# Performance work log

Measured on AMD Instinct MI355X. Metric: run time of the kernel, lower is better.

Reference implementation:

```python
import jax, jax.numpy as jnp
import numpy as np

B, IN, OUT, K = 2048, 1024, 1024, 20


def setup_inputs() -> dict:
    key = jax.random.key(0)
    k1, k2 = jax.random.split(key)
    x = jax.random.normal(k1, (B, IN), dtype=jnp.float32)
    # per-output, per-input spline coefficients: (out_features, in_features, num_knots)
    W = jax.random.normal(k2, (OUT, IN, K), dtype=jnp.float32) * 0.1
    # evenly spaced knot grid on [-2, 2] (linspace)
    knots = jnp.linspace(-2.0, 2.0, K, dtype=jnp.float32)
    return {"x": x, "W": W, "knots": knots}


def reference(x, W, knots):
    # RBF spline basis shared across all output features (this is the fusion
    # the original per-output Python loop misses):
    # basis[b, i, k] = exp(-0.5 * ((x[b, i] - knots[k]) / h)^2)
    h = knots[1] - knots[0]  # uniform knot spacing -> RBF bandwidth
    basis = jnp.exp(-0.5 * jnp.square((x[:, :, None] - knots) / h))  # (B, IN, K)
    # Each SplineLayer o computes sum_{i,k} W[o,i,k] * basis[b,i,k]; the
    # KANBlock concatenates the OUT scalars -> a single einsum.
    return jnp.einsum("bik,oik->bo", basis, W)  # (B, OUT)
```

## Files before the change

kernel.cpp:

```cpp
#include <hip/hip_runtime.h>

#define B_DIM 2048
#define IN_DIM 1024
#define OUT_DIM 1024
#define K_KNOTS 20
#define KR (IN_DIM * K_KNOTS)
#define TM 128
#define TN 128
#define BK 128
#define KSPLIT 4
#define KPB (KR / KSPLIT)
#define OUT_ELEMS (B_DIM * OUT_DIM)
#define MT_TILES (B_DIM / TM)
#define NT_TILES (OUT_DIM / TN)
#define GEMM_BLOCKS (MT_TILES * NT_TILES * KSPLIT)

#define LDS_AS0 0
#define LDS_AS1 8192
#define LDS_BS0 16384
#define LDS_BS1 24576

#define NB_QUADS (B_DIM * IN_DIM * 5)
#define NB_BASIS_BLK (NB_QUADS / 256)
#define NW4 (OUT_DIM * KR / 8)
#define NB_W_BLK (NW4 / 256)

typedef __bf16 bf16x8 __attribute__((ext_vector_type(8)));
typedef float  f32x4  __attribute__((ext_vector_type(4)));

__device__ __forceinline__ unsigned short f2bf(float f) {
    unsigned int u = __float_as_uint(f);
    unsigned int r = u + 0x7fffu + ((u >> 16) & 1u);
    return (unsigned short)(r >> 16);
}

__device__ __forceinline__ unsigned int pack2(float lo, float hi) {
    return (unsigned int)f2bf(lo) | ((unsigned int)f2bf(hi) << 16);
}

__device__ __forceinline__ void async_load16(const void* g, void* l) {
    __builtin_amdgcn_global_load_lds(
        (const __attribute__((address_space(1))) void*)g,
        (__attribute__((address_space(3))) void*)l,
        16, 0, 0);
}

__global__ void zero_out_kernel(float* out) {
    int idx = (blockIdx.x * 256 + threadIdx.x) * 4;
    float4 z = {0.f, 0.f, 0.f, 0.f};
    *(float4*)(out + idx) = z;
}

__global__ void __launch_bounds__(256) prep_kernel(
        const float* __restrict__ x,
        const float4* __restrict__ Wsrc,
        const float* __restrict__ knots,
        uint2* __restrict__ basis_out,
        uint4* __restrict__ w_out) {
    if (blockIdx.x < NB_BASIS_BLK) {
        unsigned int n = blockIdx.x * 256 + threadIdx.x;
        unsigned int q  = n % 5u;
        unsigned int bi = n / 5u;
        float t0 = knots[0];
        float h  = knots[1] - t0;
        float invh = 1.0f / h;
        float xv = x[bi];
        float k0 = (float)(4 * q);
        float v[4];
#pragma unroll
        for (int j = 0; j < 4; ++j) {
            float t = __builtin_fmaf(k0 + (float)j, h, t0);
            float d = (xv - t) * invh;
            v[j] = __expf(-0.5f * d * d);
        }
        uint2 o;
        o.x = pack2(v[0], v[1]);
        o.y = pack2(v[2], v[3]);
        basis_out[n] = o;
    } else {
        unsigned int t = (blockIdx.x - NB_BASIS_BLK) * 256 + threadIdx.x;
        float4 a = Wsrc[2 * t];
        float4 b = Wsrc[2 * t + 1];
        uint4 o;
        o.x = pack2(a.x, a.y);
        o.y = pack2(a.z, a.w);
        o.z = pack2(b.x, b.y);
        o.w = pack2(b.z, b.w);
        w_out[t] = o;
    }
}

template <int KS, bool ATOMIC>
__global__ void __launch_bounds__(256)
kan_gemm(const unsigned short* __restrict__ Ab,
         const unsigned short* __restrict__ Bb,
         float* __restrict__ out) {
    __shared__ __align__(16) unsigned short lds[32768];

    const int KPBk = KR / KS;
    const int id   = blockIdx.x;
    const int xcd  = id & 7;
    const int ord  = id >> 3;
    const int mt   = xcd * 2 + (ord & 1);
    const int nt   = (ord >> 1) & (NT_TILES - 1);
    const int z    = ord >> 4;
    const int m0 = mt * TM;
    const int n0 = nt * TN;
    const int k0 = z * KPBk;

    const int tid  = threadIdx.x;
    const int wave = tid >> 6;
    const int lane = tid & 63;
    const int wm = wave & 1;
    const int wn = wave >> 1;

    const int srow = lane >> 3;
    const int scol = ((lane & 7) ^ srow) * 8;

    f32x4 acc[4][4];
#pragma unroll
    for (int i = 0; i < 4; ++i)
#pragma unroll
        for (int j = 0; j < 4; ++j) acc[i][j] = (f32x4){0.f, 0.f, 0.f, 0.f};

    for (int kt = 0; kt < KPBk; kt += BK) {
        const int kb = k0 + kt;
        __syncthreads();
#pragma unroll
        for (int c = 0; c < 4; ++c) {
            const int chunk = wave * 4 + c;
            const int r = chunk * 8 + srow;
            const unsigned short* arow = Ab + (size_t)(m0 + r) * KR + kb + scol;
            const unsigned short* brow = Bb + (size_t)(n0 + r) * KR + kb + scol;
            unsigned short* slot = &lds[chunk * 512];
            async_load16(arow,      slot + LDS_AS0);
            async_load16(arow + 64, slot + LDS_AS1);
            async_load16(brow,      slot + LDS_BS0);
            async_load16(brow + 64, slot + LDS_BS1);
        }
        __syncthreads();

        const int quad = lane >> 4;
        const int r15  = lane & 15;
        const int r7   = lane & 7;
#pragma unroll
        for (int s = 0; s < 4; ++s) {
            const int abase = (s >> 1) ? LDS_AS1 : LDS_AS0;
            const int bbase = (s >> 1) ? LDS_BS1 : LDS_BS0;
            const int cg = (s & 1) * 4 + quad;
            const int xo = (cg ^ r7) * 8;
            bf16x8 af[4], bfv[4];
#pragma unroll
            for (int i = 0; i < 4; ++i) {
                af[i]  = *(const bf16x8*)&lds[abase + (wm * 64 + i * 16 + r15) * 64 + xo];
                bfv[i] = *(const bf16x8*)&lds[bbase + (wn * 64 + i * 16 + r15) * 64 + xo];
            }
#pragma unroll
            for (int i = 0; i < 4; ++i)
#pragma unroll
                for (int j = 0; j < 4; ++j)
                    acc[i][j] = __builtin_amdgcn_mfma_f32_16x16x32_bf16(
                        af[i], bfv[j], acc[i][j], 0, 0, 0);
        }
    }

    float* dst = ATOMIC ? out : out + (size_t)z * OUT_ELEMS;
    const int quad = lane >> 4;
    const int col  = lane & 15;
#pragma unroll
    for (int i = 0; i < 4; ++i)
#pragma unroll
        for (int j = 0; j < 4; ++j)
#pragma unroll
            for (int r = 0; r < 4; ++r) {
                const int row = m0 + wm * 64 + i * 16 + quad * 4 + r;
                const int c   = n0 + wn * 64 + j * 16 + col;
                if (ATOMIC)
                    atomicAdd(&dst[(size_t)row * OUT_DIM + c], acc[i][j][r]);
                else
                    dst[(size_t)row * OUT_DIM + c] = acc[i][j][r];
            }
}

template <int KS>
__global__ void kan_reduce(const float* __restrict__ part, float* __restrict__ out) {
    const int idx = (blockIdx.x * 256 + threadIdx.x) * 4;
    f32x4 s = *(const f32x4*)(part + idx);
#pragma unroll
    for (int z = 1; z < KS; ++z)
        s += *(const f32x4*)(part + (size_t)z * OUT_ELEMS + idx);
    *(f32x4*)(out + idx) = s;
}

__global__ void kan_fallback(const float* __restrict__ x,
                             const float* __restrict__ W,
                             const float* __restrict__ knots,
                             float* __restrict__ out) {
    __shared__ float basis[256 * K_KNOTS];
    const int b = blockIdx.x;
    const int o = blockIdx.y * blockDim.x + threadIdx.x;
    const float invh = 1.0f / (knots[1] - knots[0]);
    const float* w = W + (size_t)o * KR;
    float sum = 0.f;
    for (int i0 = 0; i0 < IN_DIM; i0 += 256) {
        __syncthreads();
        for (int idx = threadIdx.x; idx < 256 * K_KNOTS; idx += blockDim.x) {
            const int i = i0 + idx / K_KNOTS;
            const int k = idx % K_KNOTS;
            const float d = (x[(size_t)b * IN_DIM + i] - knots[k]) * invh;
            basis[idx] = __expf(-0.5f * d * d);
        }
        __syncthreads();
        for (int r = 0; r < 256 * K_KNOTS; ++r)
            sum += basis[r] * w[(size_t)i0 * K_KNOTS + r];
    }
    out[(size_t)b * OUT_DIM + o] = sum;
}

extern "C" void kernel_launch(void* const* d_in, const int* in_sizes, int n_in,
                              void* d_out, int out_size, void* d_ws, size_t ws_size,
                              hipStream_t stream) {
    const float* x     = (const float*)d_in[0];
    const float* W     = (const float*)d_in[1];
    const float* knots = (const float*)d_in[2];
    float* out = (float*)d_out;

    const size_t basis_bytes = (size_t)B_DIM * KR * 2;
    const size_t wb_bytes    = (size_t)OUT_DIM * KR * 2;
    const size_t part_bytes  = (size_t)KSPLIT * OUT_ELEMS * 4;

    unsigned short* Ab = (unsigned short*)d_ws;
    unsigned short* Bb = (unsigned short*)((char*)d_ws + basis_bytes);
    float* part = (float*)((char*)d_ws + basis_bytes + wb_bytes);

    if (ws_size >= basis_bytes + wb_bytes + part_bytes) {
        prep_kernel<<<dim3(NB_BASIS_BLK + NB_W_BLK), dim3(256), 0, stream>>>(
            x, (const float4*)W, knots, (uint2*)Ab, (uint4*)Bb);
        kan_gemm<KSPLIT, false><<<dim3(GEMM_BLOCKS), dim3(256), 0, stream>>>(Ab, Bb, part);
        kan_reduce<KSPLIT><<<dim3(OUT_ELEMS / (256 * 4)), dim3(256), 0, stream>>>(part, out);
    } else if (ws_size >= basis_bytes + wb_bytes) {
        zero_out_kernel<<<dim3(OUT_ELEMS / (256 * 4)), dim3(256), 0, stream>>>(out);
        prep_kernel<<<dim3(NB_BASIS_BLK + NB_W_BLK), dim3(256), 0, stream>>>(
            x, (const float4*)W, knots, (uint2*)Ab, (uint4*)Bb);
        kan_gemm<KSPLIT, true><<<dim3(GEMM_BLOCKS), dim3(256), 0, stream>>>(Ab, Bb, out);
    } else {
        kan_fallback<<<dim3(B_DIM, OUT_DIM / 256), dim3(256), 0, stream>>>(x, W, knots, out);
    }
}
```

Measured before the change: 254.3 us.

## Add 256x256-tile 8-wave GEMM with interleaved async staging and split-K 8

Adds a new GEMM kernel that uses 512 threads and 256x256 output tiles. It double-buffers 64-wide K slices in LDS and interleaves four async global-to-LDS stage loads with four MFMA phases per iteration, using raised wave priority and explicit waitcnt and barriers. Split-K goes from 4 to 8, giving exactly 256 blocks, and the reduce kernel now sums 8 partials. The larger tiles raise data reuse and the staging is meant to overlap loads with compute. The cost is twice the partial-sum buffer and reduce traffic, and heavy register and LDS use (128 KB LDS per block).

```diff
diff --git a/kernel.cpp b/kernel.cpp
--- a/kernel.cpp
+++ b/kernel.cpp
@@ -5,16 +5,15 @@
 #define OUT_DIM 1024
 #define K_KNOTS 20
 #define KR (IN_DIM * K_KNOTS)
+#define OUT_ELEMS (B_DIM * OUT_DIM)
+
 #define TM 128
 #define TN 128
 #define BK 128
 #define KSPLIT 4
-#define KPB (KR / KSPLIT)
-#define OUT_ELEMS (B_DIM * OUT_DIM)
 #define MT_TILES (B_DIM / TM)
 #define NT_TILES (OUT_DIM / TN)
 #define GEMM_BLOCKS (MT_TILES * NT_TILES * KSPLIT)
-
 #define LDS_AS0 0
 #define LDS_AS1 8192
 #define LDS_BS0 16384
@@ -27,6 +26,8 @@
 
 typedef __bf16 bf16x8 __attribute__((ext_vector_type(8)));
 typedef float  f32x4  __attribute__((ext_vector_type(4)));
+
+#define MFMA16(a, b, c) __builtin_amdgcn_mfma_f32_16x16x32_bf16(a, b, c, 0, 0, 0)
 
 __device__ __forceinline__ unsigned short f2bf(float f) {
     unsigned int u = __float_as_uint(f);
@@ -90,6 +91,169 @@
     }
 }
 
+#define AOFF(s, h) (((s) * 2 + (h)) * 8192)
+#define BOFF(s, h) (32768 + ((s) * 2 + (h)) * 8192)
+
+template <int KS, bool ATOMIC>
+__global__ void __launch_bounds__(512, 2)
+kan_gemm8(const unsigned short* __restrict__ Ab,
+          const unsigned short* __restrict__ Bb,
+          float* __restrict__ out) {
+    __shared__ __align__(16) unsigned short lds[65536];
+
+    constexpr int KPBk   = KR / KS;
+    constexpr int NTILES = KPBk / 64;
+
+    const int id  = blockIdx.x;
+    const int z   = id & 7;
+    const int ord = id >> 3;
+    const int mt  = ord & 7;
+    const int nt  = ord >> 3;
+    const int m0  = mt * 256;
+    const int n0  = nt * 256;
+    const int k0  = z * KPBk;
+
+    const int tid  = threadIdx.x;
+    const int wave = tid >> 6;
+    const int lane = tid & 63;
+    const int wm   = wave >> 2;
+    const int wn   = wave & 3;
+
+    const int srow8 = lane >> 3;
+    const int scol  = ((lane & 7) ^ srow8) * 8;
+
+    auto stage = [&](const unsigned short* __restrict__ src, int grow, int kb, int lbase) {
+        const unsigned short* g = src + (size_t)(grow + wave * 16 + srow8) * KR + kb + scol;
+        async_load16(g,                  &lds[lbase + wave * 1024]);
+        async_load16(g + (size_t)8 * KR, &lds[lbase + wave * 1024 + 512]);
+    };
+
+    f32x4 acc[8][4];
+#pragma unroll
+    for (int i = 0; i < 8; ++i)
+#pragma unroll
+        for (int j = 0; j < 4; ++j) acc[i][j] = (f32x4){0.f, 0.f, 0.f, 0.f};
+
+    const int q   = lane >> 4;
+    const int r15 = lane & 15;
+    const int r7  = lane & 7;
+    const int c0  = (q ^ r7) * 8;
+    const int c1  = ((4 + q) ^ r7) * 8;
+
+    stage(Ab, m0,       k0,      AOFF(0, 0));
+    stage(Ab, m0 + 128, k0,      AOFF(0, 1));
+    stage(Bb, n0,       k0,      BOFF(0, 0));
+    stage(Bb, n0 + 128, k0,      BOFF(0, 1));
+    stage(Bb, n0,       k0 + 64, BOFF(1, 0));
+    stage(Ab, m0,       k0 + 64, AOFF(1, 0));
+    asm volatile("s_waitcnt vmcnt(4)" ::: "memory");
+    __builtin_amdgcn_s_barrier();
+
+#pragma unroll 2
+    for (int t = 0; t < NTILES; ++t) {
+        const int s   = t & 1;
+        const int aB  = s * 16384 + (wm * 128 + r15) * 64;
+        const int bB  = 32768 + s * 16384 + (wn * 64 + r15) * 64;
+        const int kb1 = k0 + (t + 1) * 64;
+        const int kb2 = k0 + (t + 2) * 64;
+        bf16x8 aR[4][2], bR[4][2];
+
+#pragma unroll
+        for (int i = 0; i < 4; ++i) {
+            aR[i][0] = *(const bf16x8*)&lds[aB + i * 1024 + c0];
+            aR[i][1] = *(const bf16x8*)&lds[aB + i * 1024 + c1];
+        }
+#pragma unroll
+        for (int j = 0; j < 2; ++j) {
+            bR[j][0] = *(const bf16x8*)&lds[bB + j * 1024 + c0];
+            bR[j][1] = *(const bf16x8*)&lds[bB + j * 1024 + c1];
+        }
+        if (t + 1 < NTILES) stage(Bb, n0 + 128, kb1, BOFF(s ^ 1, 1));
+        __builtin_amdgcn_s_barrier();
+        asm volatile("s_waitcnt lgkmcnt(0)" ::: "memory");
+        __builtin_amdgcn_sched_barrier(0);
+        __builtin_amdgcn_s_setprio(1);
+#pragma unroll
+        for (int i = 0; i < 4; ++i)
+#pragma unroll
+            for (int j = 0; j < 2; ++j) {
+                acc[i][j] = MFMA16(aR[i][0], bR[j][0], acc[i][j]);
+                acc[i][j] = MFMA16(aR[i][1], bR[j][1], acc[i][j]);
+            }
+        __builtin_amdgcn_s_setprio(0);
+        __builtin_amdgcn_s_barrier();
+
+#pragma unroll
+        for (int j = 2; j < 4; ++j) {
+            bR[j][0] = *(const bf16x8*)&lds[bB + j * 1024 + c0];
+            bR[j][1] = *(const bf16x8*)&lds[bB + j * 1024 + c1];
+        }
+        if (t + 1 < NTILES) stage(Ab, m0 + 128, kb1, AOFF(s ^ 1, 1));
+        __builtin_amdgcn_s_barrier();
+        asm volatile("s_waitcnt lgkmcnt(0)" ::: "memory");
+        __builtin_amdgcn_sched_barrier(0);
+        __builtin_amdgcn_s_setprio(1);
+#pragma unroll
+        for (int i = 0; i < 4; ++i)
+#pragma unroll
+            for (int j = 2; j < 4; ++j) {
+                acc[i][j] = MFMA16(aR[i][0], bR[j][0], acc[i][j]);
+                acc[i][j] = MFMA16(aR[i][1], bR[j][1], acc[i][j]);
+            }
+        __builtin_amdgcn_s_setprio(0);
+        __builtin_amdgcn_s_barrier();
+
+#pragma unroll
+        for (int i = 0; i < 4; ++i) {
+            aR[i][0] = *(const bf16x8*)&lds[aB + (4 + i) * 1024 + c0];
+            aR[i][1] = *(const bf16x8*)&lds[aB + (4 + i) * 1024 + c1];
+        }
+        if (t + 2 < NTILES) stage(Bb, n0, kb2, BOFF(s, 0));
+        __builtin_amdgcn_s_barrier();
+        asm volatile("s_waitcnt lgkmcnt(0)" ::: "memory");
+        __builtin_amdgcn_sched_barrier(0);
+        __builtin_amdgcn_s_setprio(1);
+#pragma unroll
+        for (int i = 0; i < 4; ++i)
+#pragma unroll
+            for (int j = 2; j < 4; ++j) {
+                acc[4 + i][j] = MFMA16(aR[i][0], bR[j][0], acc[4 + i][j]);
+                acc[4 + i][j] = MFMA16(aR[i][1], bR[j][1], acc[4 + i][j]);
+            }
+        __builtin_amdgcn_s_setprio(0);
+        __builtin_amdgcn_s_barrier();
+
+        if (t + 2 < NTILES) stage(Ab, m0, kb2, AOFF(s, 0));
+        __builtin_amdgcn_s_setprio(1);
+#pragma unroll
+        for (int i = 0; i < 4; ++i)
+#pragma unroll
+            for (int j = 0; j < 2; ++j) {
+                acc[4 + i][j] = MFMA16(aR[i][0], bR[j][0], acc[4 + i][j]);
+                acc[4 + i][j] = MFMA16(aR[i][1], bR[j][1], acc[4 + i][j]);
+            }
+        __builtin_amdgcn_s_setprio(0);
+        if (t < NTILES - 2) asm volatile("s_waitcnt vmcnt(4)" ::: "memory");
+        else                asm volatile("s_waitcnt vmcnt(0)" ::: "memory");
+        __builtin_amdgcn_s_barrier();
+    }
+
+    float* dst = ATOMIC ? out : out + (size_t)z * OUT_ELEMS;
+#pragma unroll
+    for (int i = 0; i < 8; ++i)
+#pragma unroll
+        for (int j = 0; j < 4; ++j)
+#pragma unroll
+            for (int r = 0; r < 4; ++r) {
+                const int row = m0 + wm * 128 + i * 16 + q * 4 + r;
+                const int c   = n0 + wn * 64  + j * 16 + r15;
+                if (ATOMIC)
+                    atomicAdd(&dst[(size_t)row * OUT_DIM + c], acc[i][j][r]);
+                else
+                    dst[(size_t)row * OUT_DIM + c] = acc[i][j][r];
+            }
+}
+
 template <int KS, bool ATOMIC>
 __global__ void __launch_bounds__(256)
 kan_gemm(const unsigned short* __restrict__ Ab,
@@ -159,8 +323,7 @@
             for (int i = 0; i < 4; ++i)
 #pragma unroll
                 for (int j = 0; j < 4; ++j)
-                    acc[i][j] = __builtin_amdgcn_mfma_f32_16x16x32_bf16(
-                        af[i], bfv[j], acc[i][j], 0, 0, 0);
+                    acc[i][j] = MFMA16(af[i], bfv[j], acc[i][j]);
         }
     }
 
@@ -227,22 +390,28 @@
 
     const size_t basis_bytes = (size_t)B_DIM * KR * 2;
     const size_t wb_bytes    = (size_t)OUT_DIM * KR * 2;
-    const size_t part_bytes  = (size_t)KSPLIT * OUT_ELEMS * 4;
+    const size_t part8_bytes = (size_t)8 * OUT_ELEMS * 4;
+    const size_t part4_bytes = (size_t)4 * OUT_ELEMS * 4;
 
     unsigned short* Ab = (unsigned short*)d_ws;
     unsigned short* Bb = (unsigned short*)((char*)d_ws + basis_bytes);
     float* part = (float*)((char*)d_ws + basis_bytes + wb_bytes);
 
-    if (ws_size >= basis_bytes + wb_bytes + part_bytes) {
+    if (ws_size >= basis_bytes + wb_bytes + part8_bytes) {
         prep_kernel<<<dim3(NB_BASIS_BLK + NB_W_BLK), dim3(256), 0, stream>>>(
             x, (const float4*)W, knots, (uint2*)Ab, (uint4*)Bb);
-        kan_gemm<KSPLIT, false><<<dim3(GEMM_BLOCKS), dim3(256), 0, stream>>>(Ab, Bb, part);
-        kan_reduce<KSPLIT><<<dim3(OUT_ELEMS / (256 * 4)), dim3(256), 0, stream>>>(part, out);
+        kan_gemm8<8, false><<<dim3(256), dim3(512), 0, stream>>>(Ab, Bb, part);
+        kan_reduce<8><<<dim3(OUT_ELEMS / (256 * 4)), dim3(256), 0, stream>>>(part, out);
+    } else if (ws_size >= basis_bytes + wb_bytes + part4_bytes) {
+        prep_kernel<<<dim3(NB_BASIS_BLK + NB_W_BLK), dim3(256), 0, stream>>>(
+            x, (const float4*)W, knots, (uint2*)Ab, (uint4*)Bb);
+        kan_gemm<4, false><<<dim3(GEMM_BLOCKS), dim3(256), 0, stream>>>(Ab, Bb, part);
+        kan_reduce<4><<<dim3(OUT_ELEMS / (256 * 4)), dim3(256), 0, stream>>>(part, out);
     } else if (ws_size >= basis_bytes + wb_bytes) {
         zero_out_kernel<<<dim3(OUT_ELEMS / (256 * 4)), dim3(256), 0, stream>>>(out);
         prep_kernel<<<dim3(NB_BASIS_BLK + NB_W_BLK), dim3(256), 0, stream>>>(
             x, (const float4*)W, knots, (uint2*)Ab, (uint4*)Bb);
-        kan_gemm<KSPLIT, true><<<dim3(GEMM_BLOCKS), dim3(256), 0, stream>>>(Ab, Bb, out);
+        kan_gemm8<8, true><<<dim3(256), dim3(512), 0, stream>>>(Ab, Bb, out);
     } else {
         kan_fallback<<<dim3(B_DIM, OUT_DIM / 256), dim3(256), 0, stream>>>(x, W, knots, out);
     }
```

New measurement: 250.4 us. About the same (-1.5%).
